# Performance work log

Hardware: AMD Instinct MI355X
Metric: run time of the kernel (lower is better)

Reference implementation:

```python
import jax, jax.numpy as jnp
import numpy as np

B, S, D_IN = 32, 128, 17
D_PT, D_PAIR, D_OUT = 64, 128, 64
EPS = 1e-5


def _gelu(x):
    return jax.nn.gelu(x, approximate=False)  # torch nn.GELU default (erf)


def _bn(h, g, b):
    # BatchNorm1d (training mode): stats over batch and pair dims, per channel
    mean = h.mean(axis=(0, 1))
    var = h.var(axis=(0, 1))  # biased, matching torch normalization
    return (h - mean) * jax.lax.rsqrt(var + EPS) * g + b


def setup_inputs() -> dict:
    key = jax.random.key(0)
    ks = jax.random.split(key, 8)
    s = lambda k, shp, fan: jax.random.normal(k, shp, jnp.float32) * (1.0 / np.sqrt(fan))
    return {
        "x": jax.random.normal(ks[0], (B, S, D_IN), jnp.float32),
        # pointwise MLP: 17 -> 64 -> 64
        "w1": s(ks[1], (D_IN, D_PT), D_IN), "b1": jnp.zeros((D_PT,), jnp.float32),
        "w2": s(ks[2], (D_PT, D_PT), D_PT), "b2": jnp.zeros((D_PT,), jnp.float32),
        # pair MLP: 128 -> 128 -> 128 (input = 2 * D_PT)
        "wp1": s(ks[3], (2 * D_PT, D_PAIR), 2 * D_PT), "bp1": jnp.zeros((D_PAIR,), jnp.float32),
        "wp2": s(ks[4], (D_PAIR, D_PAIR), D_PAIR), "bp2": jnp.zeros((D_PAIR,), jnp.float32),
        # embed: BN(128) -> Conv1d(128,64,1) -> BN(64) -> GELU -> Conv1d(64,64,1) -> BN(64)
        "g0": jnp.ones((D_PAIR,), jnp.float32), "be0": jnp.zeros((D_PAIR,), jnp.float32),
        "wc1": s(ks[5], (D_PAIR, D_OUT), D_PAIR), "bc1": jnp.zeros((D_OUT,), jnp.float32),
        "g1": jnp.ones((D_OUT,), jnp.float32), "be1": jnp.zeros((D_OUT,), jnp.float32),
        "wc2": s(ks[6], (D_OUT, D_OUT), D_OUT), "bc2": jnp.zeros((D_OUT,), jnp.float32),
        "g2": jnp.ones((D_OUT,), jnp.float32), "be2": jnp.zeros((D_OUT,), jnp.float32),
    }


def reference(x, w1, b1, w2, b2, wp1, bp1, wp2, bp2,
              g0, be0, wc1, bc1, g1, be1, wc2, bc2, g2, be2):
    seq_len = x.shape[1]
    # pointwise MLP
    h = _gelu(x @ w1 + b1)
    h = _gelu(h @ w2 + b2)  # [B, S, D_PT]
    # tril pair gather (xi = features of particle j, xj = of particle i,
    # matching x_rep[b, a, c] = x[b, c] semantics in the torch code)
    i_idx, j_idx = jnp.tril_indices(seq_len)
    xi = h[:, j_idx, :]  # [B, P, D_PT]
    xj = h[:, i_idx, :]
    xij = jnp.concatenate([xi, xj], axis=-1)  # [B, P, 2*D_PT]
    # pair MLP
    e = _gelu(xij @ wp1 + bp1)
    e = _gelu(e @ wp2 + bp2)  # [B, P, D_PAIR]
    # embed stack (Conv1d k=1 == channel-wise linear)
    e = _bn(e, g0, be0)
    e = _gelu(_bn(e @ wc1 + bc1, g1, be1))
    e = _bn(e @ wc2 + bc2, g2, be2)  # [B, P, D_OUT]
    # symmetric scatter into dense pairwise output
    y = jnp.zeros((x.shape[0], seq_len, seq_len, e.shape[-1]), e.dtype)
    y = y.at[:, i_idx, j_idx, :].set(e)
    y = y.at[:, j_idx, i_idx, :].set(e)
    return y
```

## Files before the change

### kernel.cpp

```cpp
#include <hip/hip_runtime.h>
#include <hip/hip_bf16.h>
#include <math.h>

#define BB 32
#define SS 128
#define DIN 17
#define DPT 64
#define DPA 128
#define DOU 64
#define NP 8256
#define NROWS (BB * NP)
#define NCHUNK (NROWS / 128)
#define EPSF 1e-5f

typedef __hip_bfloat16 bf16;
typedef __attribute__((ext_vector_type(8))) short short8;
typedef __attribute__((ext_vector_type(16))) float f32x16;
typedef __attribute__((ext_vector_type(4))) float f32x4;
typedef __attribute__((ext_vector_type(4))) int int4v;
typedef __attribute__((ext_vector_type(4))) unsigned int uint4v;

#define MFMA32(a, b, c) __builtin_amdgcn_mfma_f32_32x32x16_bf16(a, b, c, 0, 0, 0)

__device__ __forceinline__ float bf2f(short u) {
    return __builtin_bit_cast(float, ((unsigned int)(unsigned short)u) << 16);
}

__device__ __forceinline__ void plswap(unsigned int& a, unsigned int& b) {
    asm("v_permlane32_swap_b32 %0, %1" : "+v"(a), "+v"(b));
}
__device__ __forceinline__ unsigned int cvtpk(float lo, float hi) {
    unsigned int r;
    asm("v_cvt_pk_bf16_f32 %0, %1, %2" : "=v"(r) : "v"(lo), "v"(hi));
    return r;
}

__device__ __forceinline__ void xform(const f32x16& a, short8& o0, short8& o1) {
    unsigned int w[8];
#pragma unroll
    for (int j = 0; j < 8; ++j) w[j] = cvtpk(a[2 * j], a[2 * j + 1]);
    plswap(w[0], w[2]);
    plswap(w[1], w[3]);
    plswap(w[4], w[6]);
    plswap(w[5], w[7]);
    uint4v u0 = {w[0], w[1], w[2], w[3]};
    uint4v u1 = {w[4], w[5], w[6], w[7]};
    o0 = __builtin_bit_cast(short8, u0);
    o1 = __builtin_bit_cast(short8, u1);
}

__device__ __forceinline__ float gelu_exact(float x) {
    float x2 = x * x;
    float m = fmaf(0.0356774081f, x2, 0.7978845608f);
    float e = __expf(2.0f * x * m);
    float r = __builtin_amdgcn_rcpf(e + 1.0f);
    return fmaf(-x, r, x);
}

__global__ void k_pairs(int* __restrict__ pairIJ) {
    int p = blockIdx.x * blockDim.x + threadIdx.x;
    if (p >= NP) return;
    int i = (int)((sqrtf(8.0f * (float)p + 1.0f) - 1.0f) * 0.5f);
    while ((i * (i + 1)) / 2 > p) --i;
    while (((i + 1) * (i + 2)) / 2 <= p) ++i;
    int j = p - (i * (i + 1)) / 2;
    pairIJ[p] = (i << 8) | j;
}

__global__ void k_pack(const float* __restrict__ wp1, const float* __restrict__ wp2,
                       const float* __restrict__ wc2, bf16* __restrict__ fragP1,
                       bf16* __restrict__ fragP2, bf16* __restrict__ fragC2) {
    int id = blockIdx.x * 256 + threadIdx.x;
    if (id < 16384) {
        int f = id >> 9, lane = (id >> 3) & 63, i = id & 7;
        int mt = f >> 3, s = f & 7;
        int k = s * 16 + (lane >> 5) * 8 + i;
        int m = mt * 32 + (lane & 31);
        fragP1[id] = __float2bfloat16(wp1[k * DPA + m]);
    } else if (id < 32768) {
        int rem = id - 16384;
        int f = rem >> 9, lane = (rem >> 3) & 63, i = rem & 7;
        int mt = f >> 3, s = f & 7;
        int k = s * 16 + (lane >> 5) * 8 + i;
        int m = mt * 32 + (lane & 31);
        fragP2[rem] = __float2bfloat16(wp2[k * DPA + m]);
    } else if (id < 36864) {
        int rem = id - 32768;
        int f = rem >> 9, lane = (rem >> 3) & 63, i = rem & 7;
        int mt = f >> 2, s = f & 3;
        int k = s * 16 + (lane >> 5) * 8 + i;
        int m = mt * 32 + (lane & 31);
        fragC2[rem] = __float2bfloat16(wc2[k * DOU + m]);
    }
}

__global__ void k_fold(const float* __restrict__ a0, const float* __restrict__ d0,
                       const float* __restrict__ wc1, const float* __restrict__ bc1,
                       bf16* __restrict__ fragC1, float* __restrict__ bc1p) {
    int id = blockIdx.x * 256 + threadIdx.x;
    if (id < 8192) {
        int f = id >> 9, lane = (id >> 3) & 63, i = id & 7;
        int mt = f >> 3, s = f & 7;
        int k = s * 16 + (lane >> 5) * 8 + i;
        int m = mt * 32 + (lane & 31);
        fragC1[id] = __float2bfloat16(a0[k] * wc1[k * DOU + m]);
    } else if (id < 8192 + 64) {
        int c = id - 8192;
        float s = bc1[c];
        for (int k = 0; k < DPA; ++k) s = fmaf(d0[k], wc1[k * DOU + c], s);
        bc1p[c] = s;
    }
}

__global__ void k_h(const float* __restrict__ x, const float* __restrict__ w1,
                    const float* __restrict__ b1, const float* __restrict__ w2,
                    const float* __restrict__ b2, bf16* __restrict__ h) {
    __shared__ float h1[4][DPT];
    int t = threadIdx.x;
    int rs = t >> 6;
    int c = t & 63;
    int r = blockIdx.x * 4 + rs;
    const float* xr = x + (size_t)r * DIN;
    float acc = b1[c];
#pragma unroll
    for (int k = 0; k < DIN; ++k) acc += xr[k] * w1[k * DPT + c];
    h1[rs][c] = gelu_exact(acc);
    __syncthreads();
    float acc2 = b2[c];
#pragma unroll
    for (int k = 0; k < DPT; ++k) acc2 += h1[rs][k] * w2[k * DPT + c];
    h[(size_t)r * DPT + c] = __float2bfloat16(gelu_exact(acc2));
}

__global__ __launch_bounds__(256, 2) void k_e0m(
    const bf16* __restrict__ h, const int* __restrict__ pairIJ,
    const short8* __restrict__ fragP1, const short8* __restrict__ fragP2,
    const float* __restrict__ bp1, const float* __restrict__ bp2,
    bf16* __restrict__ e0, float* __restrict__ part) {
    __shared__ __align__(16) char lds[49152];
    int t = threadIdx.x;
    int w = t >> 6, l = t & 63;
    int l31 = l & 31, lhi = l >> 5;
    int row0 = blockIdx.x * 128;
    int prow = w * 32 + l31;

    for (int u = t; u < 3072; u += 256) {
        short8 v = (u < 1024) ? fragP1[1024 + u] : fragP2[u - 1024];
        *(short8*)(lds + u * 16) = v;
    }

    short8 Wa[16];
#pragma unroll
    for (int i = 0; i < 16; ++i) Wa[i] = fragP1[i * 64 + l];

    int n = row0 + prow;
    int b = n / NP, p = n - b * NP;
    int ij = pairIJ[p];
    const bf16* hj = h + (((size_t)(b * SS + (ij & 255))) << 6);
    const bf16* hi = h + (((size_t)(b * SS + (ij >> 8))) << 6);
    short8 bx[8];
#pragma unroll
    for (int s = 0; s < 4; ++s) {
        bx[s] = *(const short8*)(hj + s * 16 + lhi * 8);
        bx[s + 4] = *(const short8*)(hi + s * 16 + lhi * 8);
    }
    __syncthreads();

    f32x16 acc[4];
#pragma unroll
    for (int mt = 0; mt < 4; ++mt)
#pragma unroll
        for (int g = 0; g < 4; ++g) {
            f32x4 bv = *(const f32x4*)(bp1 + mt * 32 + g * 8 + lhi * 4);
#pragma unroll
            for (int j = 0; j < 4; ++j) acc[mt][g * 4 + j] = bv[j];
        }
#pragma unroll
    for (int s = 0; s < 8; ++s) {
        short8 a2 = *(const short8*)(lds + (s * 64 + l) * 16);
        short8 a3 = *(const short8*)(lds + ((8 + s) * 64 + l) * 16);
        acc[0] = MFMA32(Wa[s], bx[s], acc[0]);
        acc[1] = MFMA32(Wa[8 + s], bx[s], acc[1]);
        acc[2] = MFMA32(a2, bx[s], acc[2]);
        acc[3] = MFMA32(a3, bx[s], acc[3]);
    }

    short8 B2[8];
#pragma unroll
    for (int mt = 0; mt < 4; ++mt) {
#pragma unroll
        for (int r = 0; r < 16; ++r) acc[mt][r] = gelu_exact(acc[mt][r]);
        xform(acc[mt], B2[2 * mt], B2[2 * mt + 1]);
    }

    f32x16 acc2[4];
#pragma unroll
    for (int mt = 0; mt < 4; ++mt)
#pragma unroll
        for (int g = 0; g < 4; ++g) {
            f32x4 bv = *(const f32x4*)(bp2 + mt * 32 + g * 8 + lhi * 4);
#pragma unroll
            for (int j = 0; j < 4; ++j) acc2[mt][g * 4 + j] = bv[j];
        }
#pragma unroll
    for (int s = 0; s < 8; ++s) {
#pragma unroll
        for (int mt = 0; mt < 4; ++mt) {
            short8 a = *(const short8*)(lds + 16384 + ((mt * 8 + s) * 64 + l) * 16);
            acc2[mt] = MFMA32(a, B2[s], acc2[mt]);
        }
    }

    short8 o[4][2];
#pragma unroll
    for (int mt = 0; mt < 4; ++mt) {
#pragma unroll
        for (int r = 0; r < 16; ++r) acc2[mt][r] = gelu_exact(acc2[mt][r]);
        xform(acc2[mt], o[mt][0], o[mt][1]);
    }
    __syncthreads();

    char* stage = lds + 16384;
#pragma unroll
    for (int mt = 0; mt < 4; ++mt) {
        int slot0 = 4 * mt + lhi, slot1 = 4 * mt + 2 + lhi;
        *(short8*)(stage + prow * 256 + ((slot0 * 16) ^ ((prow & 15) << 4))) = o[mt][0];
        *(short8*)(stage + prow * 256 + ((slot1 * 16) ^ ((prow & 15) << 4))) = o[mt][1];
    }
    __syncthreads();

    float sum[8], sq[8];
#pragma unroll
    for (int i = 0; i < 8; ++i) { sum[i] = 0.f; sq[i] = 0.f; }
    int slot = t & 15;
#pragma unroll
    for (int q = 0; q < 8; ++q) {
        int rr = (t >> 4) + 16 * q;
        short8 v = *(const short8*)(stage + rr * 256 + ((slot * 16) ^ ((rr & 15) << 4)));
        *(short8*)(e0 + (size_t)(row0 + rr) * DPA + slot * 8) = v;
#pragma unroll
        for (int i = 0; i < 8; ++i) {
            float f = bf2f(v[i]);
            sum[i] += f;
            sq[i] += f * f;
        }
    }
    __syncthreads();
    float* bb = (float*)stage;
#pragma unroll
    for (int i = 0; i < 8; ++i) {
        bb[t * 16 + i] = sum[i];
        bb[t * 16 + 8 + i] = sq[i];
    }
    __syncthreads();
    {
        int c = t & 127, isq = t >> 7;
        float s = 0.f;
#pragma unroll
        for (int g = 0; g < 16; ++g)
            s += bb[((c >> 3) + 16 * g) * 16 + isq * 8 + (c & 7)];
        part[(size_t)blockIdx.x * 256 + t] = s;
    }
}

__global__ void k_stats(const float* __restrict__ part, int nch, int nblk,
                        float* __restrict__ a, float* __restrict__ d,
                        const float* __restrict__ g, const float* __restrict__ be) {
    int c = blockIdx.x;
    __shared__ float ssum[256], ssq[256];
    float s = 0.f, q = 0.f;
    for (int bidx = threadIdx.x; bidx < nblk; bidx += 256) {
        s += part[(size_t)bidx * (2 * nch) + c];
        q += part[(size_t)bidx * (2 * nch) + nch + c];
    }
    ssum[threadIdx.x] = s;
    ssq[threadIdx.x] = q;
    __syncthreads();
    for (int w = 128; w > 0; w >>= 1) {
        if ((int)threadIdx.x < w) {
            ssum[threadIdx.x] += ssum[threadIdx.x + w];
            ssq[threadIdx.x] += ssq[threadIdx.x + w];
        }
        __syncthreads();
    }
    if (threadIdx.x == 0) {
        float mean = ssum[0] / (float)NROWS;
        float var = ssq[0] / (float)NROWS - mean * mean;
        float rstd = rsqrtf(var + EPSF);
        float aa = g[c] * rstd;
        a[c] = aa;
        d[c] = be[c] - mean * aa;
    }
}

__global__ __launch_bounds__(256) void k_e1m(
    const bf16* __restrict__ e0, const short8* __restrict__ fragC1,
    const float* __restrict__ bc1p, bf16* __restrict__ e1,
    float* __restrict__ part) {
    __shared__ __align__(16) char buf[16384];
    int t = threadIdx.x;
    int w = t >> 6, l = t & 63;
    int l31 = l & 31, lhi = l >> 5;
    int row0 = blockIdx.x * 128;
    int prow = w * 32 + l31;

    short8 Wc[16];
#pragma unroll
    for (int i = 0; i < 16; ++i) Wc[i] = fragC1[i * 64 + l];
    short8 B[8];
#pragma unroll
    for (int s = 0; s < 8; ++s)
        B[s] = *(const short8*)(e0 + (size_t)(row0 + prow) * DPA + s * 16 + lhi * 8);

    f32x16 acc[2];
#pragma unroll
    for (int mt = 0; mt < 2; ++mt)
#pragma unroll
        for (int g = 0; g < 4; ++g) {
            f32x4 bv = *(const f32x4*)(bc1p + mt * 32 + g * 8 + lhi * 4);
#pragma unroll
            for (int j = 0; j < 4; ++j) acc[mt][g * 4 + j] = bv[j];
        }
#pragma unroll
    for (int s = 0; s < 8; ++s) {
        acc[0] = MFMA32(Wc[s], B[s], acc[0]);
        acc[1] = MFMA32(Wc[8 + s], B[s], acc[1]);
    }

#pragma unroll
    for (int mt = 0; mt < 2; ++mt) {
        short8 o0, o1;
        xform(acc[mt], o0, o1);
        int slot0 = 4 * mt + lhi, slot1 = 4 * mt + 2 + lhi;
        *(short8*)(buf + prow * 128 + ((slot0 * 16) ^ ((prow & 7) << 4))) = o0;
        *(short8*)(buf + prow * 128 + ((slot1 * 16) ^ ((prow & 7) << 4))) = o1;
    }
    __syncthreads();

    float sum[8], sq[8];
#pragma unroll
    for (int i = 0; i < 8; ++i) { sum[i] = 0.f; sq[i] = 0.f; }
    int slot = t & 7;
#pragma unroll
    for (int q = 0; q < 4; ++q) {
        int rr = (t >> 3) + 32 * q;
        short8 v = *(const short8*)(buf + rr * 128 + ((slot * 16) ^ ((rr & 7) << 4)));
        *(short8*)(e1 + (size_t)(row0 + rr) * DOU + slot * 8) = v;
#pragma unroll
        for (int i = 0; i < 8; ++i) {
            float f = bf2f(v[i]);
            sum[i] += f;
            sq[i] += f * f;
        }
    }
    __syncthreads();
    float* bb = (float*)buf;
#pragma unroll
    for (int i = 0; i < 8; ++i) {
        bb[t * 16 + i] = sum[i];
        bb[t * 16 + 8 + i] = sq[i];
    }
    __syncthreads();
    if (t < 128) {
        int c = t & 63, isq = t >> 6;
        float s = 0.f;
#pragma unroll
        for (int g = 0; g < 32; ++g)
            s += bb[((c >> 3) + 8 * g) * 16 + isq * 8 + (c & 7)];
        part[(size_t)blockIdx.x * 128 + t] = s;
    }
}

__global__ __launch_bounds__(256) void k_e2m(
    const bf16* __restrict__ e1, const float* __restrict__ a1,
    const float* __restrict__ d1, const short8* __restrict__ fragC2,
    const float* __restrict__ bc2, bf16* __restrict__ e2,
    float* __restrict__ part) {
    __shared__ __align__(16) char buf[16384];
    int t = threadIdx.x;
    int w = t >> 6, l = t & 63;
    int l31 = l & 31, lhi = l >> 5;
    int row0 = blockIdx.x * 128;
    int prow = w * 32 + l31;

    short8 Wc[8];
#pragma unroll
    for (int s = 0; s < 8; ++s) Wc[s] = fragC2[s * 64 + l];

    short8 B[4];
#pragma unroll
    for (int s = 0; s < 4; ++s) {
        short8 raw = *(const short8*)(e1 + (size_t)(row0 + prow) * DOU + s * 16 + lhi * 8);
        int c0 = s * 16 + lhi * 8;
        f32x4 av0 = *(const f32x4*)(a1 + c0), av1 = *(const f32x4*)(a1 + c0 + 4);
        f32x4 dv0 = *(const f32x4*)(d1 + c0), dv1 = *(const f32x4*)(d1 + c0 + 4);
        float gg[8];
#pragma unroll
        for (int i = 0; i < 4; ++i) gg[i] = gelu_exact(fmaf(bf2f(raw[i]), av0[i], dv0[i]));
#pragma unroll
        for (int i = 0; i < 4; ++i) gg[4 + i] = gelu_exact(fmaf(bf2f(raw[4 + i]), av1[i], dv1[i]));
        uint4v u = {cvtpk(gg[0], gg[1]), cvtpk(gg[2], gg[3]),
                    cvtpk(gg[4], gg[5]), cvtpk(gg[6], gg[7])};
        B[s] = __builtin_bit_cast(short8, u);
    }

    f32x16 acc[2];
#pragma unroll
    for (int mt = 0; mt < 2; ++mt)
#pragma unroll
        for (int g = 0; g < 4; ++g) {
            f32x4 bv = *(const f32x4*)(bc2 + mt * 32 + g * 8 + lhi * 4);
#pragma unroll
            for (int j = 0; j < 4; ++j) acc[mt][g * 4 + j] = bv[j];
        }
#pragma unroll
    for (int s = 0; s < 4; ++s) {
        acc[0] = MFMA32(Wc[s], B[s], acc[0]);
        acc[1] = MFMA32(Wc[4 + s], B[s], acc[1]);
    }

#pragma unroll
    for (int mt = 0; mt < 2; ++mt) {
        short8 o0, o1;
        xform(acc[mt], o0, o1);
        int slot0 = 4 * mt + lhi, slot1 = 4 * mt + 2 + lhi;
        *(short8*)(buf + prow * 128 + ((slot0 * 16) ^ ((prow & 7) << 4))) = o0;
        *(short8*)(buf + prow * 128 + ((slot1 * 16) ^ ((prow & 7) << 4))) = o1;
    }
    __syncthreads();

    float sum[8], sq[8];
#pragma unroll
    for (int i = 0; i < 8; ++i) { sum[i] = 0.f; sq[i] = 0.f; }
    int slot = t & 7;
#pragma unroll
    for (int q = 0; q < 4; ++q) {
        int rr = (t >> 3) + 32 * q;
        short8 v = *(const short8*)(buf + rr * 128 + ((slot * 16) ^ ((rr & 7) << 4)));
        *(short8*)(e2 + (size_t)(row0 + rr) * DOU + slot * 8) = v;
#pragma unroll
        for (int i = 0; i < 8; ++i) {
            float f = bf2f(v[i]);
            sum[i] += f;
            sq[i] += f * f;
        }
    }
    __syncthreads();
    float* bb = (float*)buf;
#pragma unroll
    for (int i = 0; i < 8; ++i) {
        bb[t * 16 + i] = sum[i];
        bb[t * 16 + 8 + i] = sq[i];
    }
    __syncthreads();
    if (t < 128) {
        int c = t & 63, isq = t >> 6;
        float s = 0.f;
#pragma unroll
        for (int g = 0; g < 32; ++g)
            s += bb[((c >> 3) + 8 * g) * 16 + isq * 8 + (c & 7)];
        part[(size_t)blockIdx.x * 128 + t] = s;
    }
}

__global__ void k_out(const bf16* __restrict__ e2, const int* __restrict__ pairIJ,
                      const float* __restrict__ a2, const float* __restrict__ d2,
                      float* __restrict__ y) {
    int t = threadIdx.x;
    int n = blockIdx.x * 32 + (t >> 3);
    int c0 = (t & 7) * 8;
    int b = n / NP, p = n - b * NP;
    int ij = pairIJ[p];
    int ii = ij >> 8, jj = ij & 255;
    short8 raw = *(const short8*)(e2 + (size_t)n * DOU + c0);
    f32x4 aLo = *(const f32x4*)(a2 + c0), aHi = *(const f32x4*)(a2 + c0 + 4);
    f32x4 dLo = *(const f32x4*)(d2 + c0), dHi = *(const f32x4*)(d2 + c0 + 4);
    f32x4 v0, v1;
#pragma unroll
    for (int i = 0; i < 4; ++i) v0[i] = fmaf(bf2f(raw[i]), aLo[i], dLo[i]);
#pragma unroll
    for (int i = 0; i < 4; ++i) v1[i] = fmaf(bf2f(raw[4 + i]), aHi[i], dHi[i]);
    float* y1 = y + ((size_t)(b * SS + ii) * SS + jj) * DOU + c0;
    float* y2 = y + ((size_t)(b * SS + jj) * SS + ii) * DOU + c0;
    *(f32x4*)y1 = v0;
    *(f32x4*)(y1 + 4) = v1;
    *(f32x4*)y2 = v0;
    *(f32x4*)(y2 + 4) = v1;
}

extern "C" void kernel_launch(void* const* d_in, const int* in_sizes, int n_in,
                              void* d_out, int out_size, void* d_ws, size_t ws_size,
                              hipStream_t stream) {
    const float* x   = (const float*)d_in[0];
    const float* w1  = (const float*)d_in[1];
    const float* b1  = (const float*)d_in[2];
    const float* w2  = (const float*)d_in[3];
    const float* b2  = (const float*)d_in[4];
    const float* wp1 = (const float*)d_in[5];
    const float* bp1 = (const float*)d_in[6];
    const float* wp2 = (const float*)d_in[7];
    const float* bp2 = (const float*)d_in[8];
    const float* g0  = (const float*)d_in[9];
    const float* be0 = (const float*)d_in[10];
    const float* wc1 = (const float*)d_in[11];
    const float* bc1 = (const float*)d_in[12];
    const float* g1  = (const float*)d_in[13];
    const float* be1 = (const float*)d_in[14];
    const float* wc2 = (const float*)d_in[15];
    const float* bc2 = (const float*)d_in[16];
    const float* g2  = (const float*)d_in[17];
    const float* be2 = (const float*)d_in[18];

    char* ws = (char*)d_ws;
    const size_t OFF_PAIR   = 0;
    const size_t OFF_H      = 33280;
    const size_t OFF_PART   = 557568;
    const size_t OFF_FRAGP1 = 2671104;
    const size_t OFF_FRAGP2 = 2703872;
    const size_t OFF_FRAGC1 = 2736640;
    const size_t OFF_FRAGC2 = 2753024;
    const size_t OFF_BC1P   = 2761216;
    const size_t OFF_A0 = 2761472, OFF_D0 = 2761984;
    const size_t OFF_A1 = 2762496, OFF_D1 = 2762752;
    const size_t OFF_A2 = 2763008, OFF_D2 = 2763264;
    const size_t OFF_E2 = 2763520;

    int*   pairIJ = (int*)(ws + OFF_PAIR);
    bf16*  h      = (bf16*)(ws + OFF_H);
    float* part   = (float*)(ws + OFF_PART);
    bf16*  fragP1 = (bf16*)(ws + OFF_FRAGP1);
    bf16*  fragP2 = (bf16*)(ws + OFF_FRAGP2);
    bf16*  fragC1 = (bf16*)(ws + OFF_FRAGC1);
    bf16*  fragC2 = (bf16*)(ws + OFF_FRAGC2);
    float* bc1p   = (float*)(ws + OFF_BC1P);
    float* a0 = (float*)(ws + OFF_A0);
    float* d0 = (float*)(ws + OFF_D0);
    float* a1 = (float*)(ws + OFF_A1);
    float* d1 = (float*)(ws + OFF_D1);
    float* a2 = (float*)(ws + OFF_A2);
    float* d2 = (float*)(ws + OFF_D2);
    bf16*  e2 = (bf16*)(ws + OFF_E2);

    bf16* e0 = (bf16*)d_out;
    bf16* e1 = (bf16*)((char*)d_out + (size_t)NROWS * DPA * sizeof(bf16));
    float* y = (float*)d_out;

    k_pairs<<<(NP + 255) / 256, 256, 0, stream>>>(pairIJ);
    k_pack<<<144, 256, 0, stream>>>(wp1, wp2, wc2, fragP1, fragP2, fragC2);
    k_h<<<(BB * SS) / 4, 256, 0, stream>>>(x, w1, b1, w2, b2, h);
    k_e0m<<<NCHUNK, 256, 0, stream>>>(h, pairIJ, (const short8*)fragP1,
                                      (const short8*)fragP2, bp1, bp2, e0, part);
    k_stats<<<DPA, 256, 0, stream>>>(part, DPA, NCHUNK, a0, d0, g0, be0);
    k_fold<<<33, 256, 0, stream>>>(a0, d0, wc1, bc1, fragC1, bc1p);
    k_e1m<<<NCHUNK, 256, 0, stream>>>(e0, (const short8*)fragC1, bc1p, e1, part);
    k_stats<<<DOU, 256, 0, stream>>>(part, DOU, NCHUNK, a1, d1, g1, be1);
    k_e2m<<<NCHUNK, 256, 0, stream>>>(e1, a1, d1, (const short8*)fragC2, bc2, e2, part);
    k_stats<<<DOU, 256, 0, stream>>>(part, DOU, NCHUNK, a2, d2, g2, be2);
    k_out<<<NROWS / 32, 256, 0, stream>>>(e2, pairIJ, a2, d2, y);
}
```

Baseline: 158.1 us.

## Split pair-MLP accumulators into pairs and stage output per wave to raise occupancy

The pair-MLP kernel now computes its four 32-row MFMA output tiles two at a time and applies GELU to each pair immediately. Fewer f32x16 accumulators are live at once, which is meant to cut VGPR pressure, and the launch bound is raised from 2 to 3 blocks per CU. The output staging and the BatchNorm partial-sum buffers are now private to each wave. This drops two block-wide barriers, leaving one barrier before the final cross-wave reduction. The cost is serialised MFMA chains with less interleaving per wave, and a risk of register spills under the tighter bound.

```diff
diff --git a/kernel.cpp b/kernel.cpp
--- a/kernel.cpp
+++ b/kernel.cpp
@@ -55,6 +55,10 @@
     float e = __expf(2.0f * x * m);
     float r = __builtin_amdgcn_rcpf(e + 1.0f);
     return fmaf(-x, r, x);
+}
+__device__ __forceinline__ void gelu16(f32x16& a) {
+#pragma unroll
+    for (int r = 0; r < 16; ++r) a[r] = gelu_exact(a[r]);
 }
 
 __global__ void k_pairs(int* __restrict__ pairIJ) {
@@ -132,7 +136,7 @@
     h[(size_t)r * DPT + c] = __float2bfloat16(gelu_exact(acc2));
 }
 
-__global__ __launch_bounds__(256, 2) void k_e0m(
+__global__ __launch_bounds__(256, 3) void k_e0m(
     const bf16* __restrict__ h, const int* __restrict__ pairIJ,
     const short8* __restrict__ fragP1, const short8* __restrict__ fragP2,
     const float* __restrict__ bp1, const float* __restrict__ bp2,
@@ -166,78 +170,90 @@
     }
     __syncthreads();
 
-    f32x16 acc[4];
-#pragma unroll
-    for (int mt = 0; mt < 4; ++mt)
+    short8 B2[8];
+    {
+        f32x16 c0, c1;
 #pragma unroll
         for (int g = 0; g < 4; ++g) {
-            f32x4 bv = *(const f32x4*)(bp1 + mt * 32 + g * 8 + lhi * 4);
-#pragma unroll
-            for (int j = 0; j < 4; ++j) acc[mt][g * 4 + j] = bv[j];
-        }
-#pragma unroll
-    for (int s = 0; s < 8; ++s) {
-        short8 a2 = *(const short8*)(lds + (s * 64 + l) * 16);
-        short8 a3 = *(const short8*)(lds + ((8 + s) * 64 + l) * 16);
-        acc[0] = MFMA32(Wa[s], bx[s], acc[0]);
-        acc[1] = MFMA32(Wa[8 + s], bx[s], acc[1]);
-        acc[2] = MFMA32(a2, bx[s], acc[2]);
-        acc[3] = MFMA32(a3, bx[s], acc[3]);
-    }
-
-    short8 B2[8];
-#pragma unroll
-    for (int mt = 0; mt < 4; ++mt) {
-#pragma unroll
-        for (int r = 0; r < 16; ++r) acc[mt][r] = gelu_exact(acc[mt][r]);
-        xform(acc[mt], B2[2 * mt], B2[2 * mt + 1]);
-    }
-
-    f32x16 acc2[4];
-#pragma unroll
-    for (int mt = 0; mt < 4; ++mt)
+            f32x4 v0 = *(const f32x4*)(bp1 + 0 * 32 + g * 8 + lhi * 4);
+            f32x4 v1 = *(const f32x4*)(bp1 + 1 * 32 + g * 8 + lhi * 4);
+#pragma unroll
+            for (int j = 0; j < 4; ++j) { c0[g * 4 + j] = v0[j]; c1[g * 4 + j] = v1[j]; }
+        }
+#pragma unroll
+        for (int s = 0; s < 8; ++s) {
+            c0 = MFMA32(Wa[s], bx[s], c0);
+            c1 = MFMA32(Wa[8 + s], bx[s], c1);
+        }
+        gelu16(c0);
+        xform(c0, B2[0], B2[1]);
+        gelu16(c1);
+        xform(c1, B2[2], B2[3]);
+    }
+    {
+        f32x16 c2, c3;
 #pragma unroll
         for (int g = 0; g < 4; ++g) {
-            f32x4 bv = *(const f32x4*)(bp2 + mt * 32 + g * 8 + lhi * 4);
-#pragma unroll
-            for (int j = 0; j < 4; ++j) acc2[mt][g * 4 + j] = bv[j];
-        }
-#pragma unroll
-    for (int s = 0; s < 8; ++s) {
-#pragma unroll
-        for (int mt = 0; mt < 4; ++mt) {
-            short8 a = *(const short8*)(lds + 16384 + ((mt * 8 + s) * 64 + l) * 16);
-            acc2[mt] = MFMA32(a, B2[s], acc2[mt]);
-        }
-    }
-
-    short8 o[4][2];
-#pragma unroll
-    for (int mt = 0; mt < 4; ++mt) {
-#pragma unroll
-        for (int r = 0; r < 16; ++r) acc2[mt][r] = gelu_exact(acc2[mt][r]);
-        xform(acc2[mt], o[mt][0], o[mt][1]);
-    }
-    __syncthreads();
-
-    char* stage = lds + 16384;
+            f32x4 v0 = *(const f32x4*)(bp1 + 2 * 32 + g * 8 + lhi * 4);
+            f32x4 v1 = *(const f32x4*)(bp1 + 3 * 32 + g * 8 + lhi * 4);
+#pragma unroll
+            for (int j = 0; j < 4; ++j) { c2[g * 4 + j] = v0[j]; c3[g * 4 + j] = v1[j]; }
+        }
+#pragma unroll
+        for (int s = 0; s < 8; ++s) {
+            short8 a2 = *(const short8*)(lds + (s * 64 + l) * 16);
+            short8 a3 = *(const short8*)(lds + ((8 + s) * 64 + l) * 16);
+            c2 = MFMA32(a2, bx[s], c2);
+            c3 = MFMA32(a3, bx[s], c3);
+        }
+        gelu16(c2);
+        xform(c2, B2[4], B2[5]);
+        gelu16(c3);
+        xform(c3, B2[6], B2[7]);
+    }
+
+    short8 o[8];
+#pragma unroll
+    for (int mp = 0; mp < 2; ++mp) {
+        f32x16 c0, c1;
+#pragma unroll
+        for (int g = 0; g < 4; ++g) {
+            f32x4 v0 = *(const f32x4*)(bp2 + (2 * mp) * 32 + g * 8 + lhi * 4);
+            f32x4 v1 = *(const f32x4*)(bp2 + (2 * mp + 1) * 32 + g * 8 + lhi * 4);
+#pragma unroll
+            for (int j = 0; j < 4; ++j) { c0[g * 4 + j] = v0[j]; c1[g * 4 + j] = v1[j]; }
+        }
+#pragma unroll
+        for (int s = 0; s < 8; ++s) {
+            short8 a0 = *(const short8*)(lds + 16384 + (((2 * mp) * 8 + s) * 64 + l) * 16);
+            short8 a1 = *(const short8*)(lds + 16384 + (((2 * mp + 1) * 8 + s) * 64 + l) * 16);
+            c0 = MFMA32(a0, B2[s], c0);
+            c1 = MFMA32(a1, B2[s], c1);
+        }
+        gelu16(c0);
+        xform(c0, o[4 * mp + 0], o[4 * mp + 1]);
+        gelu16(c1);
+        xform(c1, o[4 * mp + 2], o[4 * mp + 3]);
+    }
+    __syncthreads();
+
+    char* stg = lds + 16384 + w * 8192;
 #pragma unroll
     for (int mt = 0; mt < 4; ++mt) {
         int slot0 = 4 * mt + lhi, slot1 = 4 * mt + 2 + lhi;
-        *(short8*)(stage + prow * 256 + ((slot0 * 16) ^ ((prow & 15) << 4))) = o[mt][0];
-        *(short8*)(stage + prow * 256 + ((slot1 * 16) ^ ((prow & 15) << 4))) = o[mt][1];
-    }
-    __syncthreads();
+        *(short8*)(stg + l31 * 256 + ((slot0 * 16) ^ ((l31 & 15) << 4))) = o[2 * mt];
+        *(short8*)(stg + l31 * 256 + ((slot1 * 16) ^ ((l31 & 15) << 4))) = o[2 * mt + 1];
+    }
 
     float sum[8], sq[8];
 #pragma unroll
     for (int i = 0; i < 8; ++i) { sum[i] = 0.f; sq[i] = 0.f; }
-    int slot = t & 15;
+    int slot = l & 15;
 #pragma unroll
     for (int q = 0; q < 8; ++q) {
-        int rr = (t >> 4) + 16 * q;
-        short8 v = *(const short8*)(stage + rr * 256 + ((slot * 16) ^ ((rr & 15) << 4)));
-        *(short8*)(e0 + (size_t)(row0 + rr) * DPA + slot * 8) = v;
+        int r = (l >> 4) + 4 * q;
+        short8 v = *(const short8*)(stg + r * 256 + ((slot * 16) ^ ((r & 15) << 4)));
+        *(short8*)(e0 + (size_t)(row0 + w * 32 + r) * DPA + slot * 8) = v;
 #pragma unroll
         for (int i = 0; i < 8; ++i) {
             float f = bf2f(v[i]);
@@ -245,20 +261,25 @@
             sq[i] += f * f;
         }
     }
-    __syncthreads();
-    float* bb = (float*)stage;
+
+    float* sb = (float*)stg;
 #pragma unroll
     for (int i = 0; i < 8; ++i) {
-        bb[t * 16 + i] = sum[i];
-        bb[t * 16 + 8 + i] = sq[i];
-    }
-    __syncthreads();
+        sb[l * 17 + i] = sum[i];
+        sb[l * 17 + 8 + i] = sq[i];
+    }
+    __syncthreads();
+
     {
         int c = t & 127, isq = t >> 7;
         float s = 0.f;
 #pragma unroll
-        for (int g = 0; g < 16; ++g)
-            s += bb[((c >> 3) + 16 * g) * 16 + isq * 8 + (c & 7)];
+        for (int wv = 0; wv < 4; ++wv) {
+            const float* sv = (const float*)(lds + 16384 + wv * 8192);
+#pragma unroll
+            for (int g = 0; g < 4; ++g)
+                s += sv[(g * 16 + (c >> 3)) * 17 + isq * 8 + (c & 7)];
+        }
         part[(size_t)blockIdx.x * 256 + t] = s;
     }
 }
```

Measured after the change: 158.7 us. About the same (+0.4%).
